# Kernel tuning notes

Measured on AMD Instinct MI355X. Metric: run time of the kernel, lower is better.

## Reference

```python
import jax, jax.numpy as jnp
import numpy as np

DIM = 1024
NUM_HEADS = 16
HEAD_DIM = DIM // NUM_HEADS
SCALE = HEAD_DIM ** -0.5


def setup_inputs() -> dict:
    key = jax.random.key(0)
    ks = jax.random.split(key, 6)
    B, N = 2, 2048
    s = DIM ** -0.5
    return {
        "x": jax.random.normal(ks[0], (B, N, DIM), dtype=jnp.float32),
        "Wq": jax.random.normal(ks[1], (DIM, DIM), dtype=jnp.float32) * s,
        "Wk": jax.random.normal(ks[2], (DIM, DIM), dtype=jnp.float32) * s,
        "Wv": jax.random.normal(ks[3], (DIM, DIM), dtype=jnp.float32) * s,
        "Wp": jax.random.normal(ks[4], (DIM, DIM), dtype=jnp.float32) * s,
        "bp": jax.random.normal(ks[5], (DIM,), dtype=jnp.float32) * 0.01,
    }


def reference(x, Wq, Wk, Wv, Wp, bp):
    B, N, C = x.shape
    H, D = NUM_HEADS, HEAD_DIM
    # projections (torch Linear: x @ W.T); reshape to (B, H, N, D)
    q = (x @ Wq.T).reshape(B, N, H, D).transpose(0, 2, 1, 3)
    k = (x @ Wk.T).reshape(B, N, H, D).transpose(0, 2, 1, 3)
    v = (x @ Wv.T).reshape(B, N, H, D).transpose(0, 2, 1, 3)
    attn = jnp.einsum("bhnd,bhmd->bhnm", q, k) * SCALE
    attn = jax.nn.softmax(attn, axis=-1)  # dropout p=0 -> identity
    out = jnp.einsum("bhnm,bhmd->bhnd", attn, v)
    out = out.transpose(0, 2, 1, 3).reshape(B, N, C)
    return out @ Wp.T + bp
```

## Files before the change

### kernel.cpp

```cpp
#include <hip/hip_runtime.h>
#include <cstdint>

#define DIMC   1024
#define NHEADS 16
#define HD     64
#define BATCH  2
#define SEQ    2048
#define MROWS  (BATCH*SEQ)
#define QSCALE2 0.18033688f

typedef __bf16 bf16x8 __attribute__((ext_vector_type(8)));
typedef float  f32x4  __attribute__((ext_vector_type(4)));

#define AST 88
#define TST 136

__device__ __forceinline__ unsigned short f2bf(float f) {
    union { float f; unsigned int u; } v; v.f = f;
    unsigned int u = v.u;
    u += 0x7fffu + ((u >> 16) & 1u);
    return (unsigned short)(u >> 16);
}

__device__ __forceinline__ unsigned int pk2bf(float a, float b) {
    union { float f; unsigned int u; } ua, ub;
    ua.f = a; ub.f = b;
    return __builtin_amdgcn_perm(ub.u + 0x8000u, ua.u + 0x8000u, 0x07060302u);
}

__device__ __forceinline__ void gload_lds16(const void* g, void* l) {
    __builtin_amdgcn_global_load_lds(
        (const __attribute__((address_space(1))) unsigned int*)g,
        (__attribute__((address_space(3))) unsigned int*)l, 16, 0, 0);
}

__global__ __launch_bounds__(256) void cast_all(
    const float* __restrict__ x,
    const float* __restrict__ Wq, const float* __restrict__ Wk,
    const float* __restrict__ Wv, const float* __restrict__ Wp,
    unsigned short* __restrict__ xb, unsigned short* __restrict__ Wb)
{
    const size_t M1 = (size_t)DIMC * DIMC;
    int y = blockIdx.y;
    const float* src;
    unsigned short* dst;
    if (y < 4)      { src = x  + (size_t)y * M1; dst = xb + (size_t)y * M1; }
    else if (y == 4){ src = Wq; dst = Wb; }
    else if (y == 5){ src = Wk; dst = Wb + M1; }
    else if (y == 6){ src = Wv; dst = Wb + 2 * M1; }
    else            { src = Wp; dst = Wb + 3 * M1; }
    size_t idx = ((size_t)blockIdx.x * 256 + threadIdx.x) * 4;
    float4 v = *(const float4*)(src + idx);
    ushort4 p; p.x = f2bf(v.x); p.y = f2bf(v.y); p.z = f2bf(v.z); p.w = f2bf(v.w);
    *(ushort4*)(dst + idx) = p;
}

__device__ __forceinline__ void gemm_issue(
    const unsigned short* __restrict__ A, const unsigned short* __restrict__ B,
    unsigned short* As, unsigned short* Bs, int m0, int n0, int kt)
{
    const int t = threadIdx.x;
    const int w = t >> 6, lane = t & 63;
    const int srow = lane >> 3, scol = lane & 7;
#pragma unroll
    for (int i = 0; i < 4; ++i) {
        int r  = i * 32 + w * 8 + srow;
        int cg = scol ^ (r & 7);
        gload_lds16(A + (size_t)(m0 + r) * DIMC + kt + cg * 8, As + r * 64 + scol * 8);
        gload_lds16(B + (size_t)(n0 + r) * DIMC + kt + cg * 8, Bs + r * 64 + scol * 8);
    }
}

__device__ __forceinline__ void gemm_compute(
    const unsigned short* As, const unsigned short* Bs, f32x4 acc[4][4])
{
    const int t = threadIdx.x;
    const int w = t >> 6, lane = t & 63, quad = lane >> 4, lr = lane & 15;
    const int wr = w >> 1, wc = w & 1;
#pragma unroll
    for (int kk = 0; kk < 2; ++kk) {
        bf16x8 af[4], bfr[4];
#pragma unroll
        for (int mt = 0; mt < 4; ++mt) {
            int row = wr * 64 + mt * 16 + lr;
            int cb  = kk * 4 + quad;
            af[mt] = *(const bf16x8*)&As[row * 64 + (cb ^ (row & 7)) * 8];
        }
#pragma unroll
        for (int nt = 0; nt < 4; ++nt) {
            int row = wc * 64 + nt * 16 + lr;
            int cb  = kk * 4 + quad;
            bfr[nt] = *(const bf16x8*)&Bs[row * 64 + (cb ^ (row & 7)) * 8];
        }
#pragma unroll
        for (int mt = 0; mt < 4; ++mt)
#pragma unroll
            for (int nt = 0; nt < 4; ++nt)
                acc[mt][nt] = __builtin_amdgcn_mfma_f32_16x16x32_bf16(af[mt], bfr[nt], acc[mt][nt], 0, 0, 0);
    }
}

__device__ __forceinline__ void gemm_k_loop_db(
    const unsigned short* __restrict__ A, const unsigned short* __restrict__ B,
    unsigned short* smem, int m0, int n0, f32x4 acc[4][4])
{
    unsigned short* As0 = smem;
    unsigned short* Bs0 = smem + 8192;
    unsigned short* As1 = smem + 16384;
    unsigned short* Bs1 = smem + 24576;

    gemm_issue(A, B, As0, Bs0, m0, n0, 0);
    for (int kt = 0; kt < DIMC; kt += 128) {
        __syncthreads();
        gemm_issue(A, B, As1, Bs1, m0, n0, kt + 64);
        gemm_compute(As0, Bs0, acc);
        __syncthreads();
        if (kt + 128 < DIMC) gemm_issue(A, B, As0, Bs0, m0, n0, kt + 128);
        gemm_compute(As1, Bs1, acc);
    }
}

__device__ __forceinline__ void vt_epilogue(
    unsigned short* Ts, f32x4 acc[4][4], int m0, int n0,
    unsigned short* __restrict__ vT)
{
    const int t = threadIdx.x;
    const int w = t >> 6, lane = t & 63, quad = lane >> 4, lr = lane & 15;
    const int wr = w >> 1, wc = w & 1;

    __syncthreads();
#pragma unroll
    for (int mt = 0; mt < 4; ++mt)
#pragma unroll
        for (int nt = 0; nt < 4; ++nt) {
            int lcol  = wc * 64 + nt * 16 + lr;
            int lrow0 = wr * 64 + mt * 16 + quad * 4;
            ushort4 p;
            p.x = f2bf(acc[mt][nt][0]); p.y = f2bf(acc[mt][nt][1]);
            p.z = f2bf(acc[mt][nt][2]); p.w = f2bf(acc[mt][nt][3]);
            *(ushort4*)&Ts[lcol * TST + lrow0] = p;
        }
    __syncthreads();

    int lc = t >> 1, half = t & 1;
    int cg = n0 + lc, hh = cg >> 6, dd = cg & 63;
    int bb = m0 >> 11, nn0 = m0 & (SEQ - 1);
    size_t dst = ((size_t)((bb * NHEADS + hh) * HD + dd)) * SEQ + nn0 + half * 64;
    const unsigned short* srcp = &Ts[lc * TST + half * 64];
#pragma unroll
    for (int i = 0; i < 8; ++i)
        *(uint4*)&vT[dst + i * 8] = *(const uint4*)&srcp[i * 8];
}

__global__ __launch_bounds__(256) void gemm_qkv_fast(
    const unsigned short* __restrict__ xb, const unsigned short* __restrict__ Wb,
    unsigned short* __restrict__ qo, unsigned short* __restrict__ ko,
    unsigned short* __restrict__ vT)
{
    __shared__ unsigned short smem[32768];

    const int t  = threadIdx.x;
    const int n0 = blockIdx.x * 128, m0 = blockIdx.y * 128, z = blockIdx.z;
    const unsigned short* B = Wb + (size_t)z * DIMC * DIMC;
    const int w = t >> 6, lane = t & 63, quad = lane >> 4, lr = lane & 15;
    const int wr = w >> 1, wc = w & 1;

    f32x4 acc[4][4];
#pragma unroll
    for (int mt = 0; mt < 4; ++mt)
#pragma unroll
        for (int nt = 0; nt < 4; ++nt)
#pragma unroll
            for (int r = 0; r < 4; ++r) acc[mt][nt][r] = 0.f;

    gemm_k_loop_db(xb, B, smem, m0, n0, acc);

    if (z == 2) {
        vt_epilogue(smem, acc, m0, n0, vT);
    } else {
        unsigned short* Out = (z == 0) ? qo : ko;
        const float sc = (z == 0) ? QSCALE2 : 1.0f;
#pragma unroll
        for (int mt = 0; mt < 4; ++mt)
#pragma unroll
            for (int nt = 0; nt < 4; ++nt)
#pragma unroll
                for (int r = 0; r < 4; ++r) {
                    int row = m0 + wr * 64 + mt * 16 + quad * 4 + r;
                    int col = n0 + wc * 64 + nt * 16 + lr;
                    Out[(size_t)row * DIMC + col] = f2bf(acc[mt][nt][r] * sc);
                }
    }
}

__global__ __launch_bounds__(256) void gemm_out_fast(
    const unsigned short* __restrict__ O, const unsigned short* __restrict__ Wpb,
    const float* __restrict__ bias, float* __restrict__ out)
{
    __shared__ unsigned short smem[32768];

    const int t  = threadIdx.x;
    const int n0 = blockIdx.x * 128, m0 = blockIdx.y * 128;
    const int w = t >> 6, lane = t & 63, quad = lane >> 4, lr = lane & 15;
    const int wr = w >> 1, wc = w & 1;

    f32x4 acc[4][4];
#pragma unroll
    for (int mt = 0; mt < 4; ++mt)
#pragma unroll
        for (int nt = 0; nt < 4; ++nt)
#pragma unroll
            for (int r = 0; r < 4; ++r) acc[mt][nt][r] = 0.f;

    gemm_k_loop_db(O, Wpb, smem, m0, n0, acc);

#pragma unroll
    for (int mt = 0; mt < 4; ++mt)
#pragma unroll
        for (int nt = 0; nt < 4; ++nt)
#pragma unroll
            for (int r = 0; r < 4; ++r) {
                int row = m0 + wr * 64 + mt * 16 + quad * 4 + r;
                int col = n0 + wc * 64 + nt * 16 + lr;
                out[(size_t)row * DIMC + col] = acc[mt][nt][r] + bias[col];
            }
}

__global__ __launch_bounds__(256) void attn_kernel(
    const unsigned short* __restrict__ qg, const unsigned short* __restrict__ kg,
    const unsigned short* __restrict__ vT, unsigned short* __restrict__ og)
{
    __shared__ unsigned short Ka[64 * 64];
    __shared__ unsigned short Kb[64 * 64];
    __shared__ unsigned short Va[64 * 64];
    __shared__ unsigned short Vb[64 * 64];
    __shared__ unsigned short Ps[128 * 64];

    const int t  = threadIdx.x;
    const int w = t >> 6, l = t & 63, quad = l >> 4, lr = l & 15;
    const int srow = t >> 3, scol = t & 7;
    const int pkey = (lr & 7) << 1;

    const int bid  = blockIdx.x;
    const int slot = bid >> 3;
    const int bh   = (bid & 7) * 4 + (slot >> 4);
    const int qt   = slot & 15;
    const int b    = bh >> 4, h = bh & 15;

    const unsigned short* khead = kg + ((size_t)(b * SEQ)) * DIMC + h * HD;
    const unsigned short* vhead = vT + (size_t)((b * NHEADS + h) * HD) * SEQ;

    bf16x8 qf[2][2];
#pragma unroll
    for (int mt = 0; mt < 2; ++mt) {
        const size_t qoff = ((size_t)(b * SEQ + qt * 128 + w * 32 + mt * 16 + lr)) * DIMC + h * HD;
        qf[mt][0] = *(const bf16x8*)(qg + qoff + 0  + quad * 8);
        qf[mt][1] = *(const bf16x8*)(qg + qoff + 32 + quad * 8);
    }

    bf16x8 ones;
#pragma unroll
    for (int j = 0; j < 8; ++j) ones[j] = (__bf16)1.0f;
    const f32x4 fzero = { 0.f, 0.f, 0.f, 0.f };

    f32x4 o_acc[2][4], lacc[2];
#pragma unroll
    for (int mt = 0; mt < 2; ++mt) {
        lacc[mt] = fzero;
#pragma unroll
        for (int ct = 0; ct < 4; ++ct) o_acc[mt][ct] = fzero;
    }

    auto issue = [&](int kt, unsigned short* Kd, unsigned short* Vd) {
#pragma unroll
        for (int i = 0; i < 2; ++i) {
            int r  = i * 32 + srow;
            int cg = scol ^ (r & 7);
            gload_lds16(khead + (size_t)(kt * 64 + r) * DIMC + cg * 8, Kd + r * 64 + scol * 8);
            gload_lds16(vhead + (size_t)r * SEQ + kt * 64 + cg * 8,   Vd + r * 64 + scol * 8);
        }
    };

    auto compute = [&](const unsigned short* Kc, const unsigned short* Vc) {
        f32x4 s[2][4];
#pragma unroll
        for (int nt = 0; nt < 4; ++nt) {
            int row = nt * 16 + lr;
            bf16x8 kf = *(const bf16x8*)&Kc[row * 64 + ((quad ^ (row & 7)) * 8)];
#pragma unroll
            for (int mt = 0; mt < 2; ++mt)
                s[mt][nt] = __builtin_amdgcn_mfma_f32_16x16x32_bf16(kf, qf[mt][0], fzero, 0, 0, 0);
        }
#pragma unroll
        for (int nt = 0; nt < 4; ++nt) {
            int row = nt * 16 + lr;
            bf16x8 kf = *(const bf16x8*)&Kc[row * 64 + (((4 + quad) ^ (row & 7)) * 8)];
#pragma unroll
            for (int mt = 0; mt < 2; ++mt)
                s[mt][nt] = __builtin_amdgcn_mfma_f32_16x16x32_bf16(kf, qf[mt][1], s[mt][nt], 0, 0, 0);
        }

#pragma unroll
        for (int mt = 0; mt < 2; ++mt)
#pragma unroll
            for (int nt = 0; nt < 4; ++nt) {
                uint2 pp;
                pp.x = pk2bf(__builtin_amdgcn_exp2f(s[mt][nt][0]),
                             __builtin_amdgcn_exp2f(s[mt][nt][1]));
                pp.y = pk2bf(__builtin_amdgcn_exp2f(s[mt][nt][2]),
                             __builtin_amdgcn_exp2f(s[mt][nt][3]));
                *(uint2*)&Ps[(w * 32 + mt * 16 + lr) * 64 + (((nt * 4 + quad) ^ pkey) * 4)] = pp;
            }

#pragma unroll
        for (int kk = 0; kk < 2; ++kk) {
            bf16x8 vf[4];
#pragma unroll
            for (int ct = 0; ct < 4; ++ct) {
                int row = ct * 16 + lr;
                vf[ct] = *(const bf16x8*)&Vc[row * 64 + (((kk * 4 + quad) ^ (row & 7)) * 8)];
            }
#pragma unroll
            for (int mt = 0; mt < 2; ++mt) {
                bf16x8 pf = *(const bf16x8*)&Ps[(w * 32 + mt * 16 + lr) * 64 + (((kk * 8 + quad * 2) ^ pkey) * 4)];
                lacc[mt] = __builtin_amdgcn_mfma_f32_16x16x32_bf16(pf, ones, lacc[mt], 0, 0, 0);
#pragma unroll
                for (int ct = 0; ct < 4; ++ct)
                    o_acc[mt][ct] = __builtin_amdgcn_mfma_f32_16x16x32_bf16(pf, vf[ct], o_acc[mt][ct], 0, 0, 0);
            }
        }
    };

    issue(0, Ka, Va);
    for (int kt = 0; kt < SEQ / 64; kt += 2) {
        __syncthreads();
        issue(kt + 1, Kb, Vb);
        compute(Ka, Va);

        __syncthreads();
        if (kt + 2 < SEQ / 64) issue(kt + 2, Ka, Va);
        compute(Kb, Vb);
    }

#pragma unroll
    for (int mt = 0; mt < 2; ++mt) {
        float inv[4];
#pragma unroll
        for (int r = 0; r < 4; ++r) inv[r] = 1.0f / lacc[mt][r];
#pragma unroll
        for (int ct = 0; ct < 4; ++ct)
#pragma unroll
            for (int r = 0; r < 4; ++r) {
                int qrow = qt * 128 + w * 32 + mt * 16 + quad * 4 + r;
                og[((size_t)(b * SEQ + qrow)) * DIMC + h * HD + ct * 16 + lr] =
                    f2bf(o_acc[mt][ct][r] * inv[r]);
            }
    }
}

__global__ __launch_bounds__(256) void gemm_qkv_f32(
    const float* __restrict__ x,
    const float* __restrict__ Wq, const float* __restrict__ Wk, const float* __restrict__ Wv,
    unsigned short* __restrict__ qo, unsigned short* __restrict__ ko, unsigned short* __restrict__ vT)
{
    __shared__ unsigned short smem[2 * 128 * AST];
    unsigned short* As = smem;
    unsigned short* Bs = smem + 128 * AST;

    const int t  = threadIdx.x;
    const int n0 = blockIdx.x * 128, m0 = blockIdx.y * 128, z = blockIdx.z;
    const float* W = (z == 0) ? Wq : (z == 1) ? Wk : Wv;
    const int w = t >> 6, l = t & 63, quad = l >> 4, lr = l & 15;
    const int wr = w >> 1, wc = w & 1;

    f32x4 acc[4][4];
#pragma unroll
    for (int mt = 0; mt < 4; ++mt)
#pragma unroll
        for (int nt = 0; nt < 4; ++nt)
#pragma unroll
            for (int r = 0; r < 4; ++r) acc[mt][nt][r] = 0.f;

    for (int kt = 0; kt < DIMC; kt += 64) {
        __syncthreads();
#pragma unroll
        for (int i = 0; i < 8; ++i) {
            int flat = t + i * 256;
            int row = flat >> 4, seg = flat & 15;
            float4 a = *(const float4*)(x + (size_t)(m0 + row) * DIMC + kt + seg * 4);
            ushort4 pa; pa.x = f2bf(a.x); pa.y = f2bf(a.y); pa.z = f2bf(a.z); pa.w = f2bf(a.w);
            *(ushort4*)&As[row * AST + seg * 4] = pa;
            float4 b = *(const float4*)(W + (size_t)(n0 + row) * DIMC + kt + seg * 4);
            ushort4 pb; pb.x = f2bf(b.x); pb.y = f2bf(b.y); pb.z = f2bf(b.z); pb.w = f2bf(b.w);
            *(ushort4*)&Bs[row * AST + seg * 4] = pb;
        }
        __syncthreads();
#pragma unroll
        for (int kk = 0; kk < 2; ++kk) {
            bf16x8 af[4], bfr[4];
#pragma unroll
            for (int mt = 0; mt < 4; ++mt)
                af[mt] = *(const bf16x8*)&As[(wr * 64 + mt * 16 + lr) * AST + kk * 32 + quad * 8];
#pragma unroll
            for (int nt = 0; nt < 4; ++nt)
                bfr[nt] = *(const bf16x8*)&Bs[(wc * 64 + nt * 16 + lr) * AST + kk * 32 + quad * 8];
#pragma unroll
            for (int mt = 0; mt < 4; ++mt)
#pragma unroll
                for (int nt = 0; nt < 4; ++nt)
                    acc[mt][nt] = __builtin_amdgcn_mfma_f32_16x16x32_bf16(af[mt], bfr[nt], acc[mt][nt], 0, 0, 0);
        }
    }

    if (z == 2) {
        __syncthreads();
#pragma unroll
        for (int mt = 0; mt < 4; ++mt)
#pragma unroll
            for (int nt = 0; nt < 4; ++nt) {
                int lcol  = wc * 64 + nt * 16 + lr;
                int lrow0 = wr * 64 + mt * 16 + quad * 4;
                ushort4 p;
                p.x = f2bf(acc[mt][nt][0]); p.y = f2bf(acc[mt][nt][1]);
                p.z = f2bf(acc[mt][nt][2]); p.w = f2bf(acc[mt][nt][3]);
                *(ushort4*)&smem[lcol * TST + lrow0] = p;
            }
        __syncthreads();
        int lc = t >> 1, half = t & 1;
        int cg = n0 + lc, hh = cg >> 6, dd = cg & 63;
        int bb = m0 >> 11, nn0 = m0 & (SEQ - 1);
        size_t dst = ((size_t)((bb * NHEADS + hh) * HD + dd)) * SEQ + nn0 + half * 64;
        const unsigned short* srcp = &smem[lc * TST + half * 64];
#pragma unroll
        for (int i = 0; i < 8; ++i)
            *(uint4*)&vT[dst + i * 8] = *(const uint4*)&srcp[i * 8];
    } else {
        unsigned short* Out = (z == 0) ? qo : ko;
        const float sc = (z == 0) ? QSCALE2 : 1.0f;
#pragma unroll
        for (int mt = 0; mt < 4; ++mt)
#pragma unroll
            for (int nt = 0; nt < 4; ++nt)
#pragma unroll
                for (int r = 0; r < 4; ++r) {
                    int row = m0 + wr * 64 + mt * 16 + quad * 4 + r;
                    int col = n0 + wc * 64 + nt * 16 + lr;
                    Out[(size_t)row * DIMC + col] = f2bf(acc[mt][nt][r] * sc);
                }
    }
}

__global__ __launch_bounds__(256) void gemm_out_f32(
    const unsigned short* __restrict__ A, const float* __restrict__ Wp,
    const float* __restrict__ bias, float* __restrict__ out)
{
    __shared__ unsigned short As[128 * AST];
    __shared__ unsigned short Bs[128 * AST];

    const int t  = threadIdx.x;
    const int n0 = blockIdx.x * 128, m0 = blockIdx.y * 128;
    const int w = t >> 6, l = t & 63, quad = l >> 4, lr = l & 15;
    const int wr = w >> 1, wc = w & 1;

    f32x4 acc[4][4];
#pragma unroll
    for (int mt = 0; mt < 4; ++mt)
#pragma unroll
        for (int nt = 0; nt < 4; ++nt)
#pragma unroll
            for (int r = 0; r < 4; ++r) acc[mt][nt][r] = 0.f;

    for (int kt = 0; kt < DIMC; kt += 64) {
        __syncthreads();
#pragma unroll
        for (int i = 0; i < 8; ++i) {
            int flat = t + i * 256;
            int row = flat >> 4, seg = flat & 15;
            ushort4 a = *(const ushort4*)(A + (size_t)(m0 + row) * DIMC + kt + seg * 4);
            *(ushort4*)&As[row * AST + seg * 4] = a;
            float4 b = *(const float4*)(Wp + (size_t)(n0 + row) * DIMC + kt + seg * 4);
            ushort4 pb; pb.x = f2bf(b.x); pb.y = f2bf(b.y); pb.z = f2bf(b.z); pb.w = f2bf(b.w);
            *(ushort4*)&Bs[row * AST + seg * 4] = pb;
        }
        __syncthreads();
#pragma unroll
        for (int kk = 0; kk < 2; ++kk) {
            bf16x8 af[4], bfr[4];
#pragma unroll
            for (int mt = 0; mt < 4; ++mt)
                af[mt] = *(const bf16x8*)&As[(wr * 64 + mt * 16 + lr) * AST + kk * 32 + quad * 8];
#pragma unroll
            for (int nt = 0; nt < 4; ++nt)
                bfr[nt] = *(const bf16x8*)&Bs[(wc * 64 + nt * 16 + lr) * AST + kk * 32 + quad * 8];
#pragma unroll
            for (int mt = 0; mt < 4; ++mt)
#pragma unroll
                for (int nt = 0; nt < 4; ++nt)
                    acc[mt][nt] = __builtin_amdgcn_mfma_f32_16x16x32_bf16(af[mt], bfr[nt], acc[mt][nt], 0, 0, 0);
        }
    }

#pragma unroll
    for (int mt = 0; mt < 4; ++mt)
#pragma unroll
        for (int nt = 0; nt < 4; ++nt)
#pragma unroll
            for (int r = 0; r < 4; ++r) {
                int row = m0 + wr * 64 + mt * 16 + quad * 4 + r;
                int col = n0 + wc * 64 + nt * 16 + lr;
                out[(size_t)row * DIMC + col] = acc[mt][nt][r] + bias[col];
            }
}

extern "C" void kernel_launch(void* const* d_in, const int* in_sizes, int n_in,
                              void* d_out, int out_size, void* d_ws, size_t ws_size,
                              hipStream_t stream)
{
    const float* x  = (const float*)d_in[0];
    const float* Wq = (const float*)d_in[1];
    const float* Wk = (const float*)d_in[2];
    const float* Wv = (const float*)d_in[3];
    const float* Wp = (const float*)d_in[4];
    const float* bp = (const float*)d_in[5];
    float* out = (float*)d_out;

    const size_t SZ  = (size_t)MROWS * DIMC;
    const size_t WSZ = (size_t)DIMC * DIMC;
    const size_t need = (4 * SZ + 4 * WSZ) * sizeof(unsigned short);

    if (ws_size >= need) {
        unsigned short* q  = (unsigned short*)d_ws;
        unsigned short* k  = q + SZ;
        unsigned short* vt = k + SZ;
        unsigned short* o  = vt + SZ;
        unsigned short* Wb = o + SZ;
        unsigned short* xb = (unsigned short*)d_out;

        cast_all<<<dim3(1024, 8), 256, 0, stream>>>(x, Wq, Wk, Wv, Wp, xb, Wb);
        gemm_qkv_fast<<<dim3(DIMC / 128, MROWS / 128, 3), 256, 0, stream>>>(xb, Wb, q, k, vt);
        attn_kernel<<<dim3(512), 256, 0, stream>>>(q, k, vt, o);
        gemm_out_fast<<<dim3(DIMC / 128, MROWS / 128), 256, 0, stream>>>(o, Wb + 3 * WSZ, bp, out);
    } else {
        unsigned short* q  = (unsigned short*)d_ws;
        unsigned short* k  = q + SZ;
        unsigned short* vt = k + SZ;
        unsigned short* o  = vt + SZ;

        gemm_qkv_f32<<<dim3(DIMC / 128, MROWS / 128, 3), 256, 0, stream>>>(x, Wq, Wk, Wv, q, k, vt);
        attn_kernel<<<dim3(512), 256, 0, stream>>>(q, k, vt, o);
        gemm_out_f32<<<dim3(DIMC / 128, MROWS / 128), 256, 0, stream>>>(o, Wp, bp, out);
    }
}
```

Before: 178.2 us.

## Software-pipeline attention: overlap QK^T of next tile with PV of previous

Splits the attention tile compute into S-phase, exp/store, V-register load and PV phases, and double-buffers the P tile in shared memory. The PV matmul of the previous key tile is interleaved with the QK^T matmul of the current one, so MFMA work can overlap the exp and LDS latency. V fragments are held in registers across the barrier, which raises register pressure. Launch bounds now request 2 blocks per CU, and the extra P buffer grows shared memory use.

```diff
diff --git a/kernel.cpp b/kernel.cpp
--- a/kernel.cpp
+++ b/kernel.cpp
@@ -226,7 +226,7 @@
             }
 }
 
-__global__ __launch_bounds__(256) void attn_kernel(
+__global__ __launch_bounds__(256, 2) void attn_kernel(
     const unsigned short* __restrict__ qg, const unsigned short* __restrict__ kg,
     const unsigned short* __restrict__ vT, unsigned short* __restrict__ og)
 {
@@ -234,7 +234,8 @@
     __shared__ unsigned short Kb[64 * 64];
     __shared__ unsigned short Va[64 * 64];
     __shared__ unsigned short Vb[64 * 64];
-    __shared__ unsigned short Ps[128 * 64];
+    __shared__ unsigned short PsA[128 * 64];
+    __shared__ unsigned short PsB[128 * 64];
 
     const int t  = threadIdx.x;
     const int w = t >> 6, l = t & 63, quad = l >> 4, lr = l & 15;
@@ -281,8 +282,7 @@
         }
     };
 
-    auto compute = [&](const unsigned short* Kc, const unsigned short* Vc) {
-        f32x4 s[2][4];
+    auto s_phase = [&](const unsigned short* Kc, f32x4 (&s)[2][4]) {
 #pragma unroll
         for (int nt = 0; nt < 4; ++nt) {
             int row = nt * 16 + lr;
@@ -299,7 +299,9 @@
             for (int mt = 0; mt < 2; ++mt)
                 s[mt][nt] = __builtin_amdgcn_mfma_f32_16x16x32_bf16(kf, qf[mt][1], s[mt][nt], 0, 0, 0);
         }
-
+    };
+
+    auto exp_store = [&](const f32x4 (&s)[2][4], unsigned short* PsW) {
 #pragma unroll
         for (int mt = 0; mt < 2; ++mt)
 #pragma unroll
@@ -309,38 +311,57 @@
                              __builtin_amdgcn_exp2f(s[mt][nt][1]));
                 pp.y = pk2bf(__builtin_amdgcn_exp2f(s[mt][nt][2]),
                              __builtin_amdgcn_exp2f(s[mt][nt][3]));
-                *(uint2*)&Ps[(w * 32 + mt * 16 + lr) * 64 + (((nt * 4 + quad) ^ pkey) * 4)] = pp;
-            }
-
-#pragma unroll
-        for (int kk = 0; kk < 2; ++kk) {
-            bf16x8 vf[4];
+                *(uint2*)&PsW[(w * 32 + mt * 16 + lr) * 64 + (((nt * 4 + quad) ^ pkey) * 4)] = pp;
+            }
+    };
+
+    auto vload = [&](const unsigned short* Vc, bf16x8 (&vr)[8]) {
+#pragma unroll
+        for (int kk = 0; kk < 2; ++kk)
 #pragma unroll
             for (int ct = 0; ct < 4; ++ct) {
                 int row = ct * 16 + lr;
-                vf[ct] = *(const bf16x8*)&Vc[row * 64 + (((kk * 4 + quad) ^ (row & 7)) * 8)];
-            }
+                vr[kk * 4 + ct] = *(const bf16x8*)&Vc[row * 64 + (((kk * 4 + quad) ^ (row & 7)) * 8)];
+            }
+    };
+
+    auto pv = [&](const unsigned short* PsR, const bf16x8 (&vr)[8]) {
+#pragma unroll
+        for (int kk = 0; kk < 2; ++kk)
 #pragma unroll
             for (int mt = 0; mt < 2; ++mt) {
-                bf16x8 pf = *(const bf16x8*)&Ps[(w * 32 + mt * 16 + lr) * 64 + (((kk * 8 + quad * 2) ^ pkey) * 4)];
+                bf16x8 pf = *(const bf16x8*)&PsR[(w * 32 + mt * 16 + lr) * 64 + (((kk * 8 + quad * 2) ^ pkey) * 4)];
                 lacc[mt] = __builtin_amdgcn_mfma_f32_16x16x32_bf16(pf, ones, lacc[mt], 0, 0, 0);
 #pragma unroll
                 for (int ct = 0; ct < 4; ++ct)
-                    o_acc[mt][ct] = __builtin_amdgcn_mfma_f32_16x16x32_bf16(pf, vf[ct], o_acc[mt][ct], 0, 0, 0);
-            }
-        }
+                    o_acc[mt][ct] = __builtin_amdgcn_mfma_f32_16x16x32_bf16(pf, vr[kk * 4 + ct], o_acc[mt][ct], 0, 0, 0);
+            }
     };
+
+    bf16x8 vrA[8], vrB[8];
 
     issue(0, Ka, Va);
     for (int kt = 0; kt < SEQ / 64; kt += 2) {
         __syncthreads();
         issue(kt + 1, Kb, Vb);
-        compute(Ka, Va);
-
+        {
+            f32x4 s[2][4];
+            s_phase(Ka, s);
+            if (kt) pv(PsB, vrB);
+            exp_store(s, PsA);
+            vload(Va, vrA);
+        }
         __syncthreads();
         if (kt + 2 < SEQ / 64) issue(kt + 2, Ka, Va);
-        compute(Kb, Vb);
-    }
+        {
+            f32x4 s[2][4];
+            s_phase(Kb, s);
+            pv(PsA, vrA);
+            exp_store(s, PsB);
+            vload(Vb, vrB);
+        }
+    }
+    pv(PsB, vrB);
 
 #pragma unroll
     for (int mt = 0; mt < 2; ++mt) {
```

After: 177.1 us. No clear change (-0.6%).

## Halve attention query tile and load V fragments directly from global memory

Applied to the files above, without the earlier changes.

The attention kernel now processes 64 query rows per block (16 per wave) instead of 128, doubling the grid to 1024 blocks and adding a launch-bounds occupancy hint. V tiles are no longer staged in LDS; each wave reads its V fragments straight from global memory at the start of each phase, and the shared P buffer shrinks. This cuts LDS and register use to raise occupancy and parallelism. In exchange, K and V are re-read twice as often across blocks, and the uncached direct V loads may stall the MFMA pipeline.

```diff
diff --git a/kernel.cpp b/kernel.cpp
--- a/kernel.cpp
+++ b/kernel.cpp
@@ -226,15 +226,13 @@
             }
 }
 
-__global__ __launch_bounds__(256) void attn_kernel(
+__global__ __launch_bounds__(256, 4) void attn_kernel(
     const unsigned short* __restrict__ qg, const unsigned short* __restrict__ kg,
     const unsigned short* __restrict__ vT, unsigned short* __restrict__ og)
 {
     __shared__ unsigned short Ka[64 * 64];
     __shared__ unsigned short Kb[64 * 64];
-    __shared__ unsigned short Va[64 * 64];
-    __shared__ unsigned short Vb[64 * 64];
-    __shared__ unsigned short Ps[128 * 64];
+    __shared__ unsigned short Ps[64 * 64];
 
     const int t  = threadIdx.x;
     const int w = t >> 6, l = t & 63, quad = l >> 4, lr = l & 15;
@@ -243,19 +241,18 @@
 
     const int bid  = blockIdx.x;
     const int slot = bid >> 3;
-    const int bh   = (bid & 7) * 4 + (slot >> 4);
-    const int qt   = slot & 15;
+    const int bh   = (bid & 7) * 4 + (slot >> 5);
+    const int qt   = slot & 31;
     const int b    = bh >> 4, h = bh & 15;
 
     const unsigned short* khead = kg + ((size_t)(b * SEQ)) * DIMC + h * HD;
     const unsigned short* vhead = vT + (size_t)((b * NHEADS + h) * HD) * SEQ;
 
-    bf16x8 qf[2][2];
-#pragma unroll
-    for (int mt = 0; mt < 2; ++mt) {
-        const size_t qoff = ((size_t)(b * SEQ + qt * 128 + w * 32 + mt * 16 + lr)) * DIMC + h * HD;
-        qf[mt][0] = *(const bf16x8*)(qg + qoff + 0  + quad * 8);
-        qf[mt][1] = *(const bf16x8*)(qg + qoff + 32 + quad * 8);
+    bf16x8 qf[2];
+    {
+        const size_t qoff = ((size_t)(b * SEQ + qt * 64 + w * 16 + lr)) * DIMC + h * HD;
+        qf[0] = *(const bf16x8*)(qg + qoff + 0  + quad * 8);
+        qf[1] = *(const bf16x8*)(qg + qoff + 32 + quad * 8);
     }
 
     bf16x8 ones;
@@ -263,97 +260,84 @@
     for (int j = 0; j < 8; ++j) ones[j] = (__bf16)1.0f;
     const f32x4 fzero = { 0.f, 0.f, 0.f, 0.f };
 
-    f32x4 o_acc[2][4], lacc[2];
-#pragma unroll
-    for (int mt = 0; mt < 2; ++mt) {
-        lacc[mt] = fzero;
-#pragma unroll
-        for (int ct = 0; ct < 4; ++ct) o_acc[mt][ct] = fzero;
-    }
-
-    auto issue = [&](int kt, unsigned short* Kd, unsigned short* Vd) {
+    f32x4 o_acc[4], lacc;
+    lacc = fzero;
+#pragma unroll
+    for (int ct = 0; ct < 4; ++ct) o_acc[ct] = fzero;
+
+    auto issueK = [&](int kt, unsigned short* Kd) {
 #pragma unroll
         for (int i = 0; i < 2; ++i) {
             int r  = i * 32 + srow;
             int cg = scol ^ (r & 7);
             gload_lds16(khead + (size_t)(kt * 64 + r) * DIMC + cg * 8, Kd + r * 64 + scol * 8);
-            gload_lds16(vhead + (size_t)r * SEQ + kt * 64 + cg * 8,   Vd + r * 64 + scol * 8);
         }
     };
 
-    auto compute = [&](const unsigned short* Kc, const unsigned short* Vc) {
-        f32x4 s[2][4];
+    auto phase = [&](const unsigned short* Kc, int kt) {
+        bf16x8 vf[2][4];
+#pragma unroll
+        for (int kk = 0; kk < 2; ++kk)
+#pragma unroll
+            for (int ct = 0; ct < 4; ++ct)
+                vf[kk][ct] = *(const bf16x8*)(vhead
+                    + (size_t)(ct * 16 + lr) * SEQ + kt * 64 + (kk * 4 + quad) * 8);
+
+        f32x4 s[4];
 #pragma unroll
         for (int nt = 0; nt < 4; ++nt) {
             int row = nt * 16 + lr;
             bf16x8 kf = *(const bf16x8*)&Kc[row * 64 + ((quad ^ (row & 7)) * 8)];
-#pragma unroll
-            for (int mt = 0; mt < 2; ++mt)
-                s[mt][nt] = __builtin_amdgcn_mfma_f32_16x16x32_bf16(kf, qf[mt][0], fzero, 0, 0, 0);
+            s[nt] = __builtin_amdgcn_mfma_f32_16x16x32_bf16(kf, qf[0], fzero, 0, 0, 0);
         }
 #pragma unroll
         for (int nt = 0; nt < 4; ++nt) {
             int row = nt * 16 + lr;
             bf16x8 kf = *(const bf16x8*)&Kc[row * 64 + (((4 + quad) ^ (row & 7)) * 8)];
-#pragma unroll
-            for (int mt = 0; mt < 2; ++mt)
-                s[mt][nt] = __builtin_amdgcn_mfma_f32_16x16x32_bf16(kf, qf[mt][1], s[mt][nt], 0, 0, 0);
-        }
-
-#pragma unroll
-        for (int mt = 0; mt < 2; ++mt)
-#pragma unroll
-            for (int nt = 0; nt < 4; ++nt) {
-                uint2 pp;
-                pp.x = pk2bf(__builtin_amdgcn_exp2f(s[mt][nt][0]),
-                             __builtin_amdgcn_exp2f(s[mt][nt][1]));
-                pp.y = pk2bf(__builtin_amdgcn_exp2f(s[mt][nt][2]),
-                             __builtin_amdgcn_exp2f(s[mt][nt][3]));
-                *(uint2*)&Ps[(w * 32 + mt * 16 + lr) * 64 + (((nt * 4 + quad) ^ pkey) * 4)] = pp;
-            }
+            s[nt] = __builtin_amdgcn_mfma_f32_16x16x32_bf16(kf, qf[1], s[nt], 0, 0, 0);
+        }
+
+#pragma unroll
+        for (int nt = 0; nt < 4; ++nt) {
+            uint2 pp;
+            pp.x = pk2bf(__builtin_amdgcn_exp2f(s[nt][0]),
+                         __builtin_amdgcn_exp2f(s[nt][1]));
+            pp.y = pk2bf(__builtin_amdgcn_exp2f(s[nt][2]),
+                         __builtin_amdgcn_exp2f(s[nt][3]));
+            *(uint2*)&Ps[(w * 16 + lr) * 64 + (((nt * 4 + quad) ^ pkey) * 4)] = pp;
+        }
 
 #pragma unroll
         for (int kk = 0; kk < 2; ++kk) {
-            bf16x8 vf[4];
-#pragma unroll
-            for (int ct = 0; ct < 4; ++ct) {
-                int row = ct * 16 + lr;
-                vf[ct] = *(const bf16x8*)&Vc[row * 64 + (((kk * 4 + quad) ^ (row & 7)) * 8)];
-            }
-#pragma unroll
-            for (int mt = 0; mt < 2; ++mt) {
-                bf16x8 pf = *(const bf16x8*)&Ps[(w * 32 + mt * 16 + lr) * 64 + (((kk * 8 + quad * 2) ^ pkey) * 4)];
-                lacc[mt] = __builtin_amdgcn_mfma_f32_16x16x32_bf16(pf, ones, lacc[mt], 0, 0, 0);
-#pragma unroll
-                for (int ct = 0; ct < 4; ++ct)
-                    o_acc[mt][ct] = __builtin_amdgcn_mfma_f32_16x16x32_bf16(pf, vf[ct], o_acc[mt][ct], 0, 0, 0);
-            }
+            bf16x8 pf = *(const bf16x8*)&Ps[(w * 16 + lr) * 64 + (((kk * 8 + quad * 2) ^ pkey) * 4)];
+            lacc = __builtin_amdgcn_mfma_f32_16x16x32_bf16(pf, ones, lacc, 0, 0, 0);
+#pragma unroll
+            for (int ct = 0; ct < 4; ++ct)
+                o_acc[ct] = __builtin_amdgcn_mfma_f32_16x16x32_bf16(pf, vf[kk][ct], o_acc[ct], 0, 0, 0);
         }
     };
 
-    issue(0, Ka, Va);
+    issueK(0, Ka);
     for (int kt = 0; kt < SEQ / 64; kt += 2) {
         __syncthreads();
-        issue(kt + 1, Kb, Vb);
-        compute(Ka, Va);
-
-        __syncthreads();
-        if (kt + 2 < SEQ / 64) issue(kt + 2, Ka, Va);
-        compute(Kb, Vb);
-    }
-
-#pragma unroll
-    for (int mt = 0; mt < 2; ++mt) {
+        issueK(kt + 1, Kb);
+        phase(Ka, kt);
+        __syncthreads();
+        if (kt + 2 < SEQ / 64) issueK(kt + 2, Ka);
+        phase(Kb, kt + 1);
+    }
+
+    {
         float inv[4];
 #pragma unroll
-        for (int r = 0; r < 4; ++r) inv[r] = 1.0f / lacc[mt][r];
+        for (int r = 0; r < 4; ++r) inv[r] = 1.0f / lacc[r];
 #pragma unroll
         for (int ct = 0; ct < 4; ++ct)
 #pragma unroll
             for (int r = 0; r < 4; ++r) {
-                int qrow = qt * 128 + w * 32 + mt * 16 + quad * 4 + r;
+                int qrow = qt * 64 + w * 16 + quad * 4 + r;
                 og[((size_t)(b * SEQ + qrow)) * DIMC + h * HD + ct * 16 + lr] =
-                    f2bf(o_acc[mt][ct][r] * inv[r]);
+                    f2bf(o_acc[ct][r] * inv[r]);
             }
     }
 }
@@ -538,7 +522,7 @@
 
         cast_all<<<dim3(1024, 8), 256, 0, stream>>>(x, Wq, Wk, Wv, Wp, xb, Wb);
         gemm_qkv_fast<<<dim3(DIMC / 128, MROWS / 128, 3), 256, 0, stream>>>(xb, Wb, q, k, vt);
-        attn_kernel<<<dim3(512), 256, 0, stream>>>(q, k, vt, o);
+        attn_kernel<<<dim3(1024), 256, 0, stream>>>(q, k, vt, o);
         gemm_out_fast<<<dim3(DIMC / 128, MROWS / 128), 256, 0, stream>>>(o, Wb + 3 * WSZ, bp, out);
     } else {
         unsigned short* q  = (unsigned short*)d_ws;
@@ -547,7 +531,7 @@
         unsigned short* o  = vt + SZ;
 
         gemm_qkv_f32<<<dim3(DIMC / 128, MROWS / 128, 3), 256, 0, stream>>>(x, Wq, Wk, Wv, q, k, vt);
-        attn_kernel<<<dim3(512), 256, 0, stream>>>(q, k, vt, o);
+        attn_kernel<<<dim3(1024), 256, 0, stream>>>(q, k, vt, o);
         gemm_out_f32<<<dim3(DIMC / 128, MROWS / 128), 256, 0, stream>>>(o, Wp, bp, out);
     }
 }
```

Measured after the change: 258.2 us. +44.9%, slower.
